# Kernel optimization log

Measured on AMD Instinct MI355X. Metric: run time of the kernel, lower is better.

## Reference

```python
import jax, jax.numpy as jnp
import numpy as np

IMAGE_SIZE = 256          # square render target, matches cfg.data.image_size
PIXEL_SIZE = 1.0 / 256.0  # 1/f for focal length f = image_size
T_THRESHOLD = 1e-4        # transmittance early-out threshold
ALPHA_CLIP = 0.99         # standard 3DGS per-gaussian opacity clamp
N_GAUSS = 1024


def setup_inputs() -> dict:
    key = jax.random.key(0)
    ks = jax.random.split(key, 6)
    N = N_GAUSS
    # projected 2D means in NDC-like camera plane coords, roughly [-0.5, 0.5]
    mean = jax.random.uniform(ks[0], (N, 2), dtype=jnp.float32) - 0.5
    # PSD 2x2 covariances: cov = L L^T + eps*I (typical splat footprint ~ a few pixels)
    L = jax.random.normal(ks[1], (N, 2, 2), dtype=jnp.float32) * 0.02
    cov = jnp.einsum('nij,nkj->nik', L, L) + 1e-5 * jnp.eye(2, dtype=jnp.float32)
    color = jax.random.uniform(ks[2], (N, 3), dtype=jnp.float32)
    alpha = jax.random.uniform(ks[3], (N,), dtype=jnp.float32)
    depth = jax.random.uniform(ks[4], (N,), dtype=jnp.float32) * 5.0 + 0.1
    bg = jax.random.uniform(ks[5], (IMAGE_SIZE, IMAGE_SIZE, 3), dtype=jnp.float32)
    # img_topleft = [cx/fx, cy/fy] = [0.5, 0.5] for a centered pinhole camera
    topleft = jnp.array([0.5, 0.5], dtype=jnp.float32)
    return dict(mean=mean, cov=cov, color=color, alpha=alpha, depth=depth,
                bg=bg, topleft=topleft)


def _composite(mean, cov, color, alpha, depth, bg, topleft):
    H = W = IMAGE_SIZE
    P = H * W
    # front-to-back order: sort by depth (the CUDA kernel composites depth-sorted ids)
    order = jnp.argsort(depth)
    mean = mean[order]
    cov = cov[order]
    color = color[order]
    alpha = alpha[order]
    # closed-form 2x2 inverse covariance
    a, b = cov[:, 0, 0], cov[:, 0, 1]
    c, d = cov[:, 1, 0], cov[:, 1, 1]
    det = a * d - b * c
    inv00 = d / det
    inv11 = a / det
    inv_off = -(b + c) / det  # coefficient of dx*dy in the quadratic form
    # pixel centers in camera-plane coords
    xs = (jnp.arange(W, dtype=jnp.float32) + 0.5) * PIXEL_SIZE - topleft[0]
    ys = (jnp.arange(H, dtype=jnp.float32) + 0.5) * PIXEL_SIZE - topleft[1]
    yy, xx = jnp.meshgrid(ys, xs, indexing='ij')  # [H, W]
    px = xx.reshape(P)
    py = yy.reshape(P)
    dx = px[None, :] - mean[:, 0:1]  # [N, P]
    dy = py[None, :] - mean[:, 1:2]  # [N, P]
    quad = (inv00[:, None] * dx * dx
            + inv_off[:, None] * dx * dy
            + inv11[:, None] * dy * dy)
    a_eff = jnp.clip(alpha[:, None] * jnp.exp(-0.5 * quad), 0.0, ALPHA_CLIP)  # [N, P]
    one_minus = 1.0 - a_eff
    # exclusive cumulative transmittance along the depth-sorted gaussian axis
    T_cum = jnp.cumprod(one_minus, axis=0)
    T_excl = jnp.concatenate([jnp.ones((1, P), dtype=one_minus.dtype), T_cum[:-1]], axis=0)
    # early-out: gaussians behind the point where T dropped below threshold contribute 0
    active = T_excl > T_THRESHOLD
    w = a_eff * T_excl * active  # per-gaussian per-pixel compositing weight
    img = (w.T @ color).reshape(H, W, 3)
    # final transmittance (frozen once early-out triggers)
    T_fin = jnp.prod(jnp.where(active, one_minus, 1.0), axis=0).reshape(H, W, 1)
    return img + T_fin * bg


def reference(mean, cov, color, alpha, depth, bg, topleft):
    return _composite(mean, cov, color, alpha, depth, bg, topleft)
```

## Files before the change

kernel.cpp:

```cpp
#include <hip/hip_runtime.h>
#include <hip/hip_bf16.h>

#define IMG 256
#define NG 1024
constexpr float PIX   = 1.0f / 256.0f;
constexpr float TTH   = 0.0001f;
constexpr float ACLIP = 0.99f;
constexpr float NEGHALF_LOG2E = -0.72134752044f;


__global__ __launch_bounds__(256)
void gs_prep(const float* __restrict__ mean, const float* __restrict__ cov,
             const float* __restrict__ color, const float* __restrict__ alpha,
             const float* __restrict__ depth, float* __restrict__ ws)
{
    __shared__ float sdepth[NG];
    __shared__ int   spart[4][64];
    const int tid   = threadIdx.x;
    const int lane64 = tid & 63;
    const int seg   = tid >> 6;
    const int g     = blockIdx.x * 64 + lane64;

    for (int i = tid; i < NG; i += 256) sdepth[i] = depth[i];
    __syncthreads();

    const float d = sdepth[g];
    int rank = 0;
    const float4* s4 = (const float4*)sdepth;
    const int base4 = seg * 64;
    #pragma unroll 8
    for (int k = 0; k < 64; ++k) {
        const int j4 = base4 + k;
        const float4 dj = s4[j4];
        const int j = j4 * 4;
        rank += (dj.x < d) || (dj.x == d && (j + 0) < g);
        rank += (dj.y < d) || (dj.y == d && (j + 1) < g);
        rank += (dj.z < d) || (dj.z == d && (j + 2) < g);
        rank += (dj.w < d) || (dj.w == d && (j + 3) < g);
    }
    spart[seg][lane64] = rank;
    __syncthreads();

    if (seg == 0) {
        const int r = spart[0][lane64] + spart[1][lane64]
                    + spart[2][lane64] + spart[3][lane64];

        const float a  = cov[g * 4 + 0];
        const float b  = cov[g * 4 + 1];
        const float c  = cov[g * 4 + 2];
        const float dd = cov[g * 4 + 3];
        const float det    = a * dd - b * c;
        const float inv00  = dd / det;
        const float inv11  = a / det;
        const float invoff = -(b + c) / det;

        const float al = alpha[g];
        float qcut = 2.0f * __logf(al * 1.0e6f + 1.0e-30f);
        qcut = fminf(fmaxf(qcut, 0.0f), 28.0f);
        const float rx = sqrtf(qcut * fmaxf(a,  0.0f));
        const float ry = sqrtf(qcut * fmaxf(dd, 0.0f));

        const float mx = mean[g * 2 + 0];
        const float my = mean[g * 2 + 1];

        float* o = ws + r * 12;
        o[0] = mx;
        o[1] = my;
        o[2] = inv00  * NEGHALF_LOG2E;
        o[3] = invoff * NEGHALF_LOG2E;
        o[4] = inv11  * NEGHALF_LOG2E;
        o[5] = __log2f(al + 1.0e-30f);
        o[6] = color[g * 3 + 0];
        o[7] = color[g * 3 + 1];
        o[8] = color[g * 3 + 2];
        o[9] = 0.0f; o[10] = 0.0f; o[11] = 0.0f;

        float4* bb4 = (float4*)(ws + NG * 12);
        bb4[r] = make_float4(mx, my, rx, ry);
    }
}

__global__ __launch_bounds__(512, 8)
void gs_render(const float* __restrict__ ws, const float* __restrict__ bg,
               const float* __restrict__ topleft, float* __restrict__ out)
{
    __shared__ float sC[8][4][64];
    const int tid  = threadIdx.x;
    const int wave = tid >> 6;
    const int lane = tid & 63;

    const int tile = blockIdx.x;
    const int tx = (tile & 31) * 8;
    const int ty = (tile >> 5) * 8;
    const int col = tx + (lane & 7);
    const int row = ty + (lane >> 3);
    const float tl0 = topleft[0], tl1 = topleft[1];
    const float px = ((float)col + 0.5f) * PIX - tl0;
    const float py = ((float)row + 0.5f) * PIX - tl1;
    const float cx = ((float)tx + 4.0f) * PIX - tl0;
    const float cy = ((float)ty + 4.0f) * PIX - tl1;
    const float hw = 3.5f * PIX;

    const float4* bb4 = (const float4*)(ws + NG * 12);

    float T = 1.0f, r = 0.0f, g = 0.0f, b = 0.0f;

    for (int c = 0; c < 2; ++c) {
        if (__all(T <= TTH)) break;

        const int gi = wave * 128 + c * 64 + lane;
        const float4 bb = bb4[gi];
        const bool hit = (fabsf(bb.x - cx) <= bb.z + hw) &&
                         (fabsf(bb.y - cy) <= bb.w + hw);
        unsigned long long mask = __ballot(hit);
        if (!mask) continue;

        int j = __ffsll(mask) - 1; mask &= mask - 1;
        int gg = __builtin_amdgcn_readfirstlane(wave * 128 + c * 64 + j);
        const float* gp = ws + gg * 12;
        float4 a0 = *(const float4*)(gp);
        float4 a1 = *(const float4*)(gp + 4);
        float  cb = gp[8];

        for (;;) {
            const bool more = (mask != 0);
            float4 n0, n1; float ncb = 0.0f;
            if (more) {
                const int jn = __ffsll(mask) - 1; mask &= mask - 1;
                const int g2 = __builtin_amdgcn_readfirstlane(wave * 128 + c * 64 + jn);
                const float* np = ws + g2 * 12;
                n0 = *(const float4*)(np);
                n1 = *(const float4*)(np + 4);
                ncb = np[8];
            }

            const float dx = px - a0.x;
            const float dy = py - a0.y;
            const float q  = dx * (a0.z * dx + a0.w * dy) + fmaf(a1.x, dy * dy, a1.y);
            const float aeff = fminf(exp2f(q), ACLIP);
            const float w  = aeff * T;
            r = fmaf(w, a1.z, r);
            g = fmaf(w, a1.w, g);
            b = fmaf(w, cb, b);
            T = T - w;

            if (!more) break;
            a0 = n0; a1 = n1; cb = ncb;
        }
    }

    sC[wave][0][lane] = r;
    sC[wave][1][lane] = g;
    sC[wave][2][lane] = b;
    sC[wave][3][lane] = T;
    __syncthreads();

    if (wave == 0) {
        float R = r, G = g, B = b, Tf = T;
        #pragma unroll
        for (int s = 1; s < 8; ++s) {
            R  = fmaf(Tf, sC[s][0][lane], R);
            G  = fmaf(Tf, sC[s][1][lane], G);
            B  = fmaf(Tf, sC[s][2][lane], B);
            Tf *= sC[s][3][lane];
        }

        const int p = row * 256 + col;
        const float* bgp = bg + p * 3;
        float* op = out + p * 3;
        op[0] = R + Tf * bgp[0];
        op[1] = G + Tf * bgp[1];
        op[2] = B + Tf * bgp[2];
    }
}

extern "C" void kernel_launch(void* const* d_in, const int* in_sizes, int n_in,
                              void* d_out, int out_size, void* d_ws, size_t ws_size,
                              hipStream_t stream) {
    const float* mean    = (const float*)d_in[0];
    const float* cov     = (const float*)d_in[1];
    const float* color   = (const float*)d_in[2];
    const float* alpha   = (const float*)d_in[3];
    const float* depth   = (const float*)d_in[4];
    const float* bg      = (const float*)d_in[5];
    const float* topleft = (const float*)d_in[6];
    float* out = (float*)d_out;
    float* ws  = (float*)d_ws;

    gs_prep<<<16, 256, 0, stream>>>(mean, cov, color, alpha, depth, ws);
    gs_render<<<1024, 512, 0, stream>>>(ws, bg, topleft, out);
}
```

Measured before the change: 81.41 us.

## Widen depth-rank prep, hoist bbox ballots, tighten cutoff, tree-reduce wave partials

The depth-ranking prep kernel now uses 512 threads, so each wave scans half as many depths. The render kernel loads and ballots both bounding-box chunks up front and drops the per-chunk transmittance early-out check. The footprint cutoff is tightened (alpha*1e5, qcut capped at 24), which shrinks the boxes and culls more gaussians. The final per-wave compositing becomes a two-level reduction through an extra shared buffer and barrier. The tighter cutoff trades a little accuracy for fewer gaussians evaluated per pixel.

```diff
diff --git a/kernel.cpp b/kernel.cpp
--- a/kernel.cpp
+++ b/kernel.cpp
@@ -9,27 +9,27 @@
 constexpr float NEGHALF_LOG2E = -0.72134752044f;
 
 
-__global__ __launch_bounds__(256)
+__global__ __launch_bounds__(512)
 void gs_prep(const float* __restrict__ mean, const float* __restrict__ cov,
              const float* __restrict__ color, const float* __restrict__ alpha,
              const float* __restrict__ depth, float* __restrict__ ws)
 {
     __shared__ float sdepth[NG];
-    __shared__ int   spart[4][64];
-    const int tid   = threadIdx.x;
+    __shared__ int   spart[8][64];
+    const int tid    = threadIdx.x;
     const int lane64 = tid & 63;
-    const int seg   = tid >> 6;
-    const int g     = blockIdx.x * 64 + lane64;
-
-    for (int i = tid; i < NG; i += 256) sdepth[i] = depth[i];
+    const int seg    = tid >> 6;
+    const int g      = blockIdx.x * 64 + lane64;
+
+    for (int i = tid; i < NG; i += 512) sdepth[i] = depth[i];
     __syncthreads();
 
     const float d = sdepth[g];
     int rank = 0;
     const float4* s4 = (const float4*)sdepth;
-    const int base4 = seg * 64;
+    const int base4 = seg * 32;
     #pragma unroll 8
-    for (int k = 0; k < 64; ++k) {
+    for (int k = 0; k < 32; ++k) {
         const int j4 = base4 + k;
         const float4 dj = s4[j4];
         const int j = j4 * 4;
@@ -42,8 +42,9 @@
     __syncthreads();
 
     if (seg == 0) {
-        const int r = spart[0][lane64] + spart[1][lane64]
-                    + spart[2][lane64] + spart[3][lane64];
+        int r = 0;
+        #pragma unroll
+        for (int s = 0; s < 8; ++s) r += spart[s][lane64];
 
         const float a  = cov[g * 4 + 0];
         const float b  = cov[g * 4 + 1];
@@ -55,8 +56,8 @@
         const float invoff = -(b + c) / det;
 
         const float al = alpha[g];
-        float qcut = 2.0f * __logf(al * 1.0e6f + 1.0e-30f);
-        qcut = fminf(fmaxf(qcut, 0.0f), 28.0f);
+        float qcut = 2.0f * __logf(al * 1.0e5f + 1.0e-30f);
+        qcut = fminf(fmaxf(qcut, 0.0f), 24.0f);
         const float rx = sqrtf(qcut * fmaxf(a,  0.0f));
         const float ry = sqrtf(qcut * fmaxf(dd, 0.0f));
 
@@ -85,6 +86,7 @@
                const float* __restrict__ topleft, float* __restrict__ out)
 {
     __shared__ float sC[8][4][64];
+    __shared__ float sP[2][4][64];
     const int tid  = threadIdx.x;
     const int wave = tid >> 6;
     const int lane = tid & 63;
@@ -103,20 +105,27 @@
 
     const float4* bb4 = (const float4*)(ws + NG * 12);
 
+    const int g0 = wave * 128 + lane;
+    const float4 bbA = bb4[g0];
+    const float4 bbB = bb4[g0 + 64];
+
+    const bool hitA = (fabsf(bbA.x - cx) <= bbA.z + hw) &&
+                      (fabsf(bbA.y - cy) <= bbA.w + hw);
+    const bool hitB = (fabsf(bbB.x - cx) <= bbB.z + hw) &&
+                      (fabsf(bbB.y - cy) <= bbB.w + hw);
+    unsigned long long maskA = __ballot(hitA);
+    unsigned long long maskB = __ballot(hitB);
+
     float T = 1.0f, r = 0.0f, g = 0.0f, b = 0.0f;
 
+    #pragma unroll
     for (int c = 0; c < 2; ++c) {
-        if (__all(T <= TTH)) break;
-
-        const int gi = wave * 128 + c * 64 + lane;
-        const float4 bb = bb4[gi];
-        const bool hit = (fabsf(bb.x - cx) <= bb.z + hw) &&
-                         (fabsf(bb.y - cy) <= bb.w + hw);
-        unsigned long long mask = __ballot(hit);
+        unsigned long long mask = c ? maskB : maskA;
         if (!mask) continue;
+        const int cbase = wave * 128 + c * 64;
 
         int j = __ffsll(mask) - 1; mask &= mask - 1;
-        int gg = __builtin_amdgcn_readfirstlane(wave * 128 + c * 64 + j);
+        int gg = __builtin_amdgcn_readfirstlane(cbase + j);
         const float* gp = ws + gg * 12;
         float4 a0 = *(const float4*)(gp);
         float4 a1 = *(const float4*)(gp + 4);
@@ -127,7 +136,7 @@
             float4 n0, n1; float ncb = 0.0f;
             if (more) {
                 const int jn = __ffsll(mask) - 1; mask &= mask - 1;
-                const int g2 = __builtin_amdgcn_readfirstlane(wave * 128 + c * 64 + jn);
+                const int g2 = __builtin_amdgcn_readfirstlane(cbase + jn);
                 const float* np = ws + g2 * 12;
                 n0 = *(const float4*)(np);
                 n1 = *(const float4*)(np + 4);
@@ -155,15 +164,31 @@
     sC[wave][3][lane] = T;
     __syncthreads();
 
+    if (wave < 2) {
+        const int s0 = wave * 4;
+        float R = sC[s0][0][lane], G = sC[s0][1][lane],
+              B = sC[s0][2][lane], Tf = sC[s0][3][lane];
+        #pragma unroll
+        for (int s = 1; s < 4; ++s) {
+            R  = fmaf(Tf, sC[s0 + s][0][lane], R);
+            G  = fmaf(Tf, sC[s0 + s][1][lane], G);
+            B  = fmaf(Tf, sC[s0 + s][2][lane], B);
+            Tf *= sC[s0 + s][3][lane];
+        }
+        sP[wave][0][lane] = R;
+        sP[wave][1][lane] = G;
+        sP[wave][2][lane] = B;
+        sP[wave][3][lane] = Tf;
+    }
+    __syncthreads();
+
     if (wave == 0) {
-        float R = r, G = g, B = b, Tf = T;
-        #pragma unroll
-        for (int s = 1; s < 8; ++s) {
-            R  = fmaf(Tf, sC[s][0][lane], R);
-            G  = fmaf(Tf, sC[s][1][lane], G);
-            B  = fmaf(Tf, sC[s][2][lane], B);
-            Tf *= sC[s][3][lane];
-        }
+        const float R0 = sP[0][0][lane], G0 = sP[0][1][lane],
+                    B0 = sP[0][2][lane], T0 = sP[0][3][lane];
+        const float R  = fmaf(T0, sP[1][0][lane], R0);
+        const float G  = fmaf(T0, sP[1][1][lane], G0);
+        const float B  = fmaf(T0, sP[1][2][lane], B0);
+        const float Tf = T0 * sP[1][3][lane];
 
         const int p = row * 256 + col;
         const float* bgp = bg + p * 3;
@@ -187,6 +212,6 @@
     float* out = (float*)d_out;
     float* ws  = (float*)d_ws;
 
-    gs_prep<<<16, 256, 0, stream>>>(mean, cov, color, alpha, depth, ws);
+    gs_prep<<<16, 512, 0, stream>>>(mean, cov, color, alpha, depth, ws);
     gs_render<<<1024, 512, 0, stream>>>(ws, bg, topleft, out);
 }
```

Result: faster. 77.17 us (-5.2%).
